# Performance work log

Measured on AMD Instinct MI355X. Metric: run time of the kernel, lower is better.

The kernel has to match this reference:

```python
import jax, jax.numpy as jnp
import numpy as np

EPS = 1e-06
GROUPS = ((0, 16), (16, 32), (32, 64))


def setup_inputs() -> dict:
    key = jax.random.key(0)
    k1, k2, k3 = jax.random.split(key, 3)
    B, C, H, W = 32, 64, 128, 128
    x = jax.random.normal(k1, (B, C, H, W), dtype=jnp.float32)
    # stands in for Beta(0.1, 0.1) sample in the torch module
    lmda = jax.random.uniform(k2, (B, 1, 1, 1), dtype=jnp.float32)
    perm = jax.random.permutation(k3, B).astype(jnp.int32)
    return {"x": x, "lmda": lmda, "perm": perm}


def _lower_median(a, axis):
    # torch.median returns the lower of the two middle values for even n
    n = a.shape[axis]
    s = jnp.sort(a, axis=axis)
    return jax.lax.slice_in_dim(s, (n - 1) // 2, (n - 1) // 2 + 1, axis=axis)


def _group_mix(xg, lmda, perm):
    B, Cg, H, W = xg.shape
    mu = jax.lax.stop_gradient(jnp.mean(xg, axis=(2, 3), keepdims=True))
    var = jnp.var(xg, axis=(2, 3), keepdims=True, ddof=1)  # torch unbiased var
    sig = jax.lax.stop_gradient(jnp.sqrt(var + EPS))
    x_normed = (xg - mu) / sig

    med = jax.lax.stop_gradient(_lower_median(_lower_median(xg, 2), 3))  # [B,Cg,1,1]

    flat = xg.reshape(B, Cg, H * W)
    gram = jnp.einsum('bci,bdi->bcd', flat, flat) / (H * W + EPS)
    gram = jax.lax.stop_gradient(gram) + (0.001 + 1e-06) * jnp.eye(Cg, dtype=xg.dtype)

    w, v = jnp.linalg.eigh(gram)
    inv_sqrt = 1.0 / jnp.sqrt(w + EPS)
    whitening = jnp.einsum('bij,bj,bkj->bik', v, inv_sqrt, v)  # [B,Cg,Cg]

    xw = jnp.einsum('bcd,bdn->bcn', whitening, flat - mu.reshape(B, Cg, 1))
    xw = xw.reshape(B, Cg, H, W)

    gram_mix = xw * lmda + xw[perm] * (1.0 - lmda)
    med_mix = med * lmda + med[perm] * (1.0 - lmda)
    return x_normed * gram_mix + med_mix


def reference(x, lmda, perm):
    outs = [_group_mix(x[:, s:e], lmda, perm) for s, e in GROUPS]
    return jnp.concatenate(outs, axis=1)
```

## Files before the change

### kernel.cpp

```cpp
#include <hip/hip_runtime.h>
#include <hip/hip_fp16.h>

#define HWPIX 16384

typedef _Float16 h2 __attribute__((ext_vector_type(2)));
typedef int v2i __attribute__((ext_vector_type(2)));
typedef float f2 __attribute__((ext_vector_type(2)));
typedef float f4 __attribute__((ext_vector_type(4)));


#define TPAD 130

template<int J>
__device__ inline unsigned shfl_xor_u(unsigned v, int lane) {
  if constexpr (J == 1)
    return (unsigned)__builtin_amdgcn_mov_dpp((int)v, 0xB1, 0xF, 0xF, true);
  else if constexpr (J == 2)
    return (unsigned)__builtin_amdgcn_mov_dpp((int)v, 0x4E, 0xF, 0xF, true);
  else if constexpr (J == 4)
    return (unsigned)__builtin_amdgcn_ds_swizzle((int)v, 0x101F);
  else if constexpr (J == 8)
    return (unsigned)__builtin_amdgcn_ds_swizzle((int)v, 0x201F);
  else if constexpr (J == 16)
    return (unsigned)__builtin_amdgcn_ds_swizzle((int)v, 0x401F);
  else {
#if __has_builtin(__builtin_amdgcn_permlane32_swap)
    v2i r = __builtin_amdgcn_permlane32_swap((int)v, (int)v, false, false);
    return (lane & 32) ? (unsigned)r[0] : (unsigned)r[1];
#else
    return (unsigned)__shfl_xor((int)v, 32);
#endif
  }
}

__device__ inline unsigned pk_min(unsigned a, unsigned b) {
  h2 x = __builtin_bit_cast(h2, a), y = __builtin_bit_cast(h2, b);
  return __builtin_bit_cast(unsigned, __builtin_elementwise_min(x, y));
}
__device__ inline unsigned pk_max(unsigned a, unsigned b) {
  h2 x = __builtin_bit_cast(h2, a), y = __builtin_bit_cast(h2, b);
  return __builtin_bit_cast(unsigned, __builtin_elementwise_max(x, y));
}

template<int CTRL>
__device__ inline unsigned dppmax(unsigned m) {
  unsigned t = (unsigned)__builtin_amdgcn_update_dpp((int)m, (int)m, CTRL, 0xF, 0xF, false);
  return pk_max(m, t);
}

template<int K, int J, int Q>
__device__ inline void bstep(unsigned (&v0)[Q], unsigned (&v1)[Q], const int lane) {
  const bool sel0 = (((lane & J) == 0) == ((lane & K) == 0));
  const int i1 = lane + 64;
  const bool sel1 = (((i1 & J) == 0) == ((i1 & K) == 0));
  unsigned pv[Q];
  #pragma unroll
  for (int q = 0; q < Q; ++q) pv[q] = shfl_xor_u<J>(v0[q], lane);
  #pragma unroll
  for (int q = 0; q < Q; ++q)
    v0[q] = sel0 ? pk_min(v0[q], pv[q]) : pk_max(v0[q], pv[q]);
  #pragma unroll
  for (int q = 0; q < Q; ++q) pv[q] = shfl_xor_u<J>(v1[q], lane);
  #pragma unroll
  for (int q = 0; q < Q; ++q)
    v1[q] = sel1 ? pk_min(v1[q], pv[q]) : pk_max(v1[q], pv[q]);
  if constexpr (J > 1) bstep<K, J / 2, Q>(v0, v1, lane);
}

template<int Q>
__device__ inline void median128h_low(unsigned (&v0)[Q], unsigned (&v1)[Q],
                                      unsigned (&m)[Q], const int lane) {
  bstep<2, 1, Q>(v0, v1, lane);
  bstep<4, 2, Q>(v0, v1, lane);
  bstep<8, 4, Q>(v0, v1, lane);
  bstep<16, 8, Q>(v0, v1, lane);
  bstep<32, 16, Q>(v0, v1, lane);
  bstep<64, 32, Q>(v0, v1, lane);
  #pragma unroll
  for (int q = 0; q < Q; ++q) m[q] = pk_min(v0[q], v1[q]);
  #pragma unroll
  for (int q = 0; q < Q; ++q) m[q] = dppmax<0x111>(m[q]);
  #pragma unroll
  for (int q = 0; q < Q; ++q) m[q] = dppmax<0x112>(m[q]);
  #pragma unroll
  for (int q = 0; q < Q; ++q) m[q] = dppmax<0x114>(m[q]);
  #pragma unroll
  for (int q = 0; q < Q; ++q) m[q] = dppmax<0x118>(m[q]);
  #pragma unroll
  for (int q = 0; q < Q; ++q) m[q] = dppmax<0x142>(m[q]);
  #pragma unroll
  for (int q = 0; q < Q; ++q) m[q] = dppmax<0x143>(m[q]);
}

template<int CTRL>
__device__ inline float fmax_dpp(float m) {
  float t = __builtin_bit_cast(float,
      __builtin_amdgcn_update_dpp(__builtin_bit_cast(int, m),
                                  __builtin_bit_cast(int, m), CTRL, 0xF, 0xF, false));
  return fmaxf(m, t);
}

__device__ inline float median128f_low(float v0, float v1, const int lane) {
  #pragma unroll
  for (int k = 2; k <= 64; k <<= 1) {
    #pragma unroll
    for (int j = k >> 1; j > 0; j >>= 1) {
      const bool sel0 = (((lane & j) == 0) == ((lane & k) == 0));
      const int i1 = lane + 64;
      const bool sel1 = (((i1 & j) == 0) == ((i1 & k) == 0));
      float pv = __shfl_xor(v0, j);
      v0 = sel0 ? fminf(v0, pv) : fmaxf(v0, pv);
      float pw = __shfl_xor(v1, j);
      v1 = sel1 ? fminf(v1, pw) : fmaxf(v1, pw);
    }
  }
  float m = fminf(v0, v1);
  m = fmax_dpp<0x111>(m); m = fmax_dpp<0x112>(m); m = fmax_dpp<0x114>(m);
  m = fmax_dpp<0x118>(m); m = fmax_dpp<0x142>(m); m = fmax_dpp<0x143>(m);
  return m;
}

__global__ __launch_bounds__(512) void stats_kernel(const float* __restrict__ x,
                                                    float* __restrict__ med) {
  __shared__ __half tile[128 * TPAD];
  __shared__ float colmed[128];

  const int bc = blockIdx.x;
  const int tid = threadIdx.x;
  const float* xp = x + (size_t)bc * HWPIX;

  #pragma unroll
  for (int j = 0; j < 8; ++j) {
    int v = tid + j * 512;
    int h = v >> 5;
    int w = (v & 31) * 4;
    float4 val = *reinterpret_cast<const float4*>(xp + (size_t)v * 4);
    __half2* dst = reinterpret_cast<__half2*>(&tile[h * TPAD + w]);
    dst[0] = __floats2half2_rn(val.x, val.y);
    dst[1] = __floats2half2_rn(val.z, val.w);
  }
  __syncthreads();

  const int lane = tid & 63;
  const int wid  = tid >> 6;
  {
    const int w = wid * 16;
    unsigned v0[8], v1[8], m[8];
    #pragma unroll
    for (int q = 0; q < 8; ++q) {
      v0[q] = *reinterpret_cast<const unsigned*>(&tile[lane * TPAD + w + 2 * q]);
      v1[q] = *reinterpret_cast<const unsigned*>(&tile[(lane + 64) * TPAD + w + 2 * q]);
    }
    median128h_low<8>(v0, v1, m, lane);
    if (lane == 63) {
      #pragma unroll
      for (int q = 0; q < 8; ++q) {
        h2 mv = __builtin_bit_cast(h2, m[q]);
        colmed[w + 2 * q]     = (float)mv.x;
        colmed[w + 2 * q + 1] = (float)mv.y;
      }
    }
  }
  __syncthreads();
  if (wid == 0) {
    float m = median128f_low(colmed[lane], colmed[lane + 64], lane);
    if (lane == 63) med[bc] = m;
  }
}

template<int CG>
__global__ __launch_bounds__(256) void gram_kernel(const float* __restrict__ x,
                                                   float* __restrict__ gpart,
                                                   float* __restrict__ rspart) {
  constexpr int QT   = CG / 4;
  constexpr int TPG  = QT * QT;
  constexpr int PQ   = 256 / TPG;
  constexpr int SUBP = 256 / PQ;
  constexpr int THR  = 256 / CG;
  __shared__ float tile[CG][260];

  const int b = blockIdx.z;
  const int g = blockIdx.y;
  const int s    = (CG == 16) ? g * 16  : 32;
  const int goff = (CG == 16) ? g * 256 : 512;
  const int chunk = blockIdx.x;
  const int k0 = chunk * 1024;
  const int tid = threadIdx.x;
  const int pq = tid / TPG;
  const int t  = tid % TPG;
  const int ty = t / QT, tx = t % QT;
  const int r0 = ty * 4, c0 = tx * 4;
  const int rrow = tid / THR;
  const int rseg = tid % THR;

  const float* xb = x + (((size_t)(b * 64 + s)) << 14) + k0;
  float acc[4][4] = {};
  float rsum = 0.f;

  for (int sc = 0; sc < 4; ++sc) {
    #pragma unroll
    for (int v = tid; v < CG * 64; v += 256) {
      int r = v >> 6;
      int p4 = (v & 63) * 4;
      *reinterpret_cast<float4*>(&tile[r][p4]) =
          *reinterpret_cast<const float4*>(xb + ((size_t)r << 14) + sc * 256 + p4);
    }
    __syncthreads();
    const int pb0 = pq * SUBP;
    #pragma unroll
    for (int p = pb0; p < pb0 + SUBP; p += 4) {
      float4 a[4], bb[4];
      #pragma unroll
      for (int i = 0; i < 4; ++i) a[i]  = *reinterpret_cast<const float4*>(&tile[r0 + i][p]);
      #pragma unroll
      for (int i = 0; i < 4; ++i) bb[i] = *reinterpret_cast<const float4*>(&tile[c0 + i][p]);
      #pragma unroll
      for (int i = 0; i < 4; ++i)
        #pragma unroll
        for (int j = 0; j < 4; ++j)
          acc[i][j] += a[i].x * bb[j].x + a[i].y * bb[j].y +
                       a[i].z * bb[j].z + a[i].w * bb[j].w;
    }
    #pragma unroll
    for (int i = 0; i < CG / 4; ++i) {
      const float4 v = *reinterpret_cast<const float4*>(&tile[rrow][rseg * CG + i * 4]);
      rsum += v.x + v.y + v.z + v.w;
    }
    __syncthreads();
  }

  #pragma unroll
  for (int j = 1; j < THR; j <<= 1) rsum += __shfl_xor(rsum, j);
  if (rseg == 0) rspart[chunk * 2048 + b * 64 + s + rrow] = rsum;

  float* scratch = reinterpret_cast<float*>(tile);
  #pragma unroll
  for (int i = 0; i < 4; ++i)
    #pragma unroll
    for (int j = 0; j < 4; ++j)
      scratch[(t * PQ + pq) * 16 + i * 4 + j] = acc[i][j];
  __syncthreads();
  if (pq == 0) {
    float* gp = gpart + (size_t)(chunk * 32 + b) * 1536 + goff;
    #pragma unroll
    for (int i = 0; i < 4; ++i)
      #pragma unroll
      for (int j = 0; j < 4; ++j) {
        float v = 0.f;
        for (int q = 0; q < PQ; ++q) v += scratch[(t * PQ + q) * 16 + i * 4 + j];
        gp[(r0 + i) * CG + (c0 + j)] = v;
      }
  }
}

template<int CG>
__device__ __forceinline__ void ns_impl(const float* __restrict__ gpart,
                                        const float* __restrict__ rspart,
                                        float* __restrict__ mu,
                                        float* __restrict__ rsig,
                                        float* __restrict__ wht,
                                        const int b, const int g, char* smem) {
  constexpr int NE = CG * CG;
  constexpr int PADC = CG + 4;
  constexpr int MS = CG * PADC;
  float* Y0 = (float*)smem;
  float* Z0 = Y0 + MS;
  float* Y1 = Z0 + MS;
  float* Z1 = Y1 + MS;
  float* T  = Z1 + MS;
  float* red = T + MS;

  const int s    = (CG == 16) ? g * 16  : 32;
  const int goff = (CG == 16) ? g * 256 : 512;
  const int tid = threadIdx.x;
  const float invHW = (float)(1.0 / (16384.0 + 1e-6));

  for (int e = tid; e < NE; e += 256) {
    int r = e / CG, c = e % CG;
    float v = 0.f;
    #pragma unroll
    for (int ch = 0; ch < 16; ++ch)
      v += gpart[(size_t)(ch * 32 + b) * 1536 + goff + e];
    T[r * PADC + c] = v;
  }
  __syncthreads();

  if (tid < CG) {
    float rs = 0.f;
    #pragma unroll
    for (int ch = 0; ch < 16; ++ch) rs += rspart[ch * 2048 + b * 64 + s + tid];
    const float diag = T[tid * PADC + tid];
    const float mean = rs * (1.0f / HWPIX);
    const float var = (diag - rs * mean) / (float)(HWPIX - 1);
    mu[b * 64 + s + tid] = mean;
    rsig[b * 64 + s + tid] = rsqrtf(var + 1e-6f);
  }
  __syncthreads();

  float ssq = 0.f;
  for (int e = tid; e < NE; e += 256) {
    int r = e / CG, c = e % CG;
    float v = T[r * PADC + c] * invHW + ((r == c) ? 0.001002f : 0.0f);
    T[r * PADC + c] = v;
    ssq += v * v;
  }
  red[tid] = ssq;
  __syncthreads();
  for (int off = 128; off > 0; off >>= 1) {
    if (tid < off) red[tid] += red[tid + off];
    __syncthreads();
  }
  const float cn = sqrtf(red[0]);
  const float icn = 1.0f / cn;
  for (int e = tid; e < NE; e += 256) {
    int r = e / CG, c = e % CG;
    Y0[r * PADC + c] = T[r * PADC + c] * icn;
    Z0[r * PADC + c] = (r == c) ? 1.0f : 0.0f;
  }
  __syncthreads();

  constexpr int ACT = NE / 4;
  const int r  = tid / (CG / 4);
  const int c0 = (tid % (CG / 4)) * 4;

  for (int it = 0; it < 12; ++it) {
    float* Yi = (it & 1) ? Y1 : Y0;
    float* Zi = (it & 1) ? Z1 : Z0;
    float* Yo = (it & 1) ? Y0 : Y1;
    float* Zo = (it & 1) ? Z0 : Z1;
    if (tid < ACT) {
      float ax = 0.f, ay = 0.f, az = 0.f, aw = 0.f;
      #pragma unroll
      for (int k = 0; k < CG; ++k) {
        float zr = Zi[r * PADC + k];
        const float4 yk = *reinterpret_cast<const float4*>(&Yi[k * PADC + c0]);
        ax += zr * yk.x; ay += zr * yk.y; az += zr * yk.z; aw += zr * yk.w;
      }
      float4 tv;
      tv.x = ((r == c0 + 0) ? 3.f : 0.f) - ax;
      tv.y = ((r == c0 + 1) ? 3.f : 0.f) - ay;
      tv.z = ((r == c0 + 2) ? 3.f : 0.f) - az;
      tv.w = ((r == c0 + 3) ? 3.f : 0.f) - aw;
      *reinterpret_cast<float4*>(&T[r * PADC + c0]) = tv;
    }
    __syncthreads();
    if (tid < ACT) {
      float yx = 0.f, yy = 0.f, yz = 0.f, yw = 0.f;
      float zx = 0.f, zy = 0.f, zz = 0.f, zw = 0.f;
      #pragma unroll
      for (int k = 0; k < CG; ++k) {
        float yr = Yi[r * PADC + k];
        float tr = T[r * PADC + k];
        const float4 tk = *reinterpret_cast<const float4*>(&T[k * PADC + c0]);
        const float4 zk = *reinterpret_cast<const float4*>(&Zi[k * PADC + c0]);
        yx += yr * tk.x; yy += yr * tk.y; yz += yr * tk.z; yw += yr * tk.w;
        zx += tr * zk.x; zy += tr * zk.y; zz += tr * zk.z; zw += tr * zk.w;
      }
      *reinterpret_cast<float4*>(&Yo[r * PADC + c0]) =
          make_float4(0.5f * yx, 0.5f * yy, 0.5f * yz, 0.5f * yw);
      *reinterpret_cast<float4*>(&Zo[r * PADC + c0]) =
          make_float4(0.5f * zx, 0.5f * zy, 0.5f * zz, 0.5f * zw);
    }
    __syncthreads();
  }

  const float wscale = rsqrtf(cn);
  for (int e = tid; e < NE; e += 256) {
    int r2 = e / CG, c2 = e % CG;
    wht[b * 1536 + goff + e] = Z0[r2 * PADC + c2] * wscale;
  }
}

__global__ __launch_bounds__(256) void ns_all(const float* __restrict__ gpart,
                                              const float* __restrict__ rspart,
                                              float* __restrict__ mu,
                                              float* __restrict__ rsig,
                                              float* __restrict__ wht) {
  __shared__ __align__(16) char smem[5 * 32 * 36 * 4 + 1024];
  const int bid = blockIdx.x;
  if (bid < 64) ns_impl<16>(gpart, rspart, mu, rsig, wht, bid >> 1, bid & 1, smem);
  else          ns_impl<32>(gpart, rspart, mu, rsig, wht, bid - 64, 0, smem);
}

__global__ __launch_bounds__(256, 2) void apply16(
    const float* __restrict__ x, const float* __restrict__ lmda,
    const int* __restrict__ perm, const float* __restrict__ mu,
    const float* __restrict__ rsig, const float* __restrict__ med,
    const float* __restrict__ wht, float* __restrict__ out) {
  __shared__ float W1[256], W2[256];
  __shared__ float mu1[16], mu2[16], rs1[16], mm[16];

  const int b = blockIdx.z;
  const int g = blockIdx.y;
  const int s = g * 16, goff = g * 256;
  const int tid = threadIdx.x;
  const int pb = perm[b];
  const float lam = lmda[b];
  const float oml = 1.0f - lam;

  if (tid < 256) {
    W1[tid] = wht[b  * 1536 + goff + tid] * lam;
    W2[tid] = wht[pb * 1536 + goff + tid] * oml;
  }
  if (tid < 16) {
    int ch1 = b * 64 + s + tid, ch2 = pb * 64 + s + tid;
    mu1[tid] = mu[ch1];
    mu2[tid] = mu[ch2];
    rs1[tid] = rsig[ch1];
    mm[tid]  = lam * med[ch1] + oml * med[ch2];
  }
  __syncthreads();

  const int p = blockIdx.x * 1024 + tid * 4;
  const float* xb1 = x + (((size_t)(b  * 64 + s)) << 14) + p;
  const float* xb2 = x + (((size_t)(pb * 64 + s)) << 14) + p;
  float* ob = out + (((size_t)(b * 64 + s)) << 14) + p;

  f4 xv1[16], xv2[16];
  #pragma unroll
  for (int d = 0; d < 16; ++d) xv1[d] = *reinterpret_cast<const f4*>(xb1 + ((size_t)d << 14));
  #pragma unroll
  for (int d = 0; d < 16; ++d) xv2[d] = *reinterpret_cast<const f4*>(xb2 + ((size_t)d << 14));
  #pragma unroll
  for (int d = 0; d < 16; ++d) { xv1[d] -= mu1[d]; xv2[d] -= mu2[d]; }

  f4 acc[16] = {};
  #pragma unroll
  for (int d = 0; d < 16; ++d) {
    #pragma unroll
    for (int c = 0; c < 16; ++c) {
      acc[c] += W1[d * 16 + c] * xv1[d];
      acc[c] += W2[d * 16 + c] * xv2[d];
    }
  }
  #pragma unroll
  for (int c = 0; c < 16; ++c) {
    f4 v = xv1[c] * rs1[c] * acc[c] + mm[c];
    __builtin_nontemporal_store(v, reinterpret_cast<f4*>(ob + ((size_t)c << 14)));
  }
}

__global__ __launch_bounds__(256, 2) void apply32(
    const float* __restrict__ x, const float* __restrict__ lmda,
    const int* __restrict__ perm, const float* __restrict__ mu,
    const float* __restrict__ rsig, const float* __restrict__ med,
    const float* __restrict__ wht, float* __restrict__ out) {
  __shared__ float W1[1024], W2[1024];
  __shared__ float mu1[32], mu2[32], rs1[32], mm[32];

  const int b = blockIdx.z;
  const int tid = threadIdx.x;
  const int pb = perm[b];
  const float lam = lmda[b];
  const float oml = 1.0f - lam;

  for (int e = tid; e < 1024; e += 256) {
    W1[e] = wht[b  * 1536 + 512 + e] * lam;
    W2[e] = wht[pb * 1536 + 512 + e] * oml;
  }
  if (tid < 32) {
    int ch1 = b * 64 + 32 + tid, ch2 = pb * 64 + 32 + tid;
    mu1[tid] = mu[ch1];
    mu2[tid] = mu[ch2];
    rs1[tid] = rsig[ch1];
    mm[tid]  = lam * med[ch1] + oml * med[ch2];
  }
  __syncthreads();

  const int p = blockIdx.x * 512 + tid * 2;
  const float* xb1 = x + (((size_t)(b  * 64 + 32)) << 14) + p;
  const float* xb2 = x + (((size_t)(pb * 64 + 32)) << 14) + p;
  float* ob = out + (((size_t)(b * 64 + 32)) << 14) + p;

  f2 xv1[32], xv2[32];
  #pragma unroll
  for (int d = 0; d < 32; ++d) xv1[d] = *reinterpret_cast<const f2*>(xb1 + ((size_t)d << 14));
  #pragma unroll
  for (int d = 0; d < 32; ++d) xv2[d] = *reinterpret_cast<const f2*>(xb2 + ((size_t)d << 14));
  #pragma unroll
  for (int d = 0; d < 32; ++d) { xv1[d] -= mu1[d]; xv2[d] -= mu2[d]; }

  f2 acc[32] = {};
  #pragma unroll
  for (int d = 0; d < 32; ++d) {
    #pragma unroll
    for (int c = 0; c < 32; ++c) {
      acc[c] += W1[d * 32 + c] * xv1[d];
      acc[c] += W2[d * 32 + c] * xv2[d];
    }
  }
  #pragma unroll
  for (int c = 0; c < 32; ++c) {
    f2 v = xv1[c] * rs1[c] * acc[c] + mm[c];
    __builtin_nontemporal_store(v, reinterpret_cast<f2*>(ob + ((size_t)c << 14)));
  }
}

extern "C" void kernel_launch(void* const* d_in, const int* in_sizes, int n_in,
                              void* d_out, int out_size, void* d_ws, size_t ws_size,
                              hipStream_t stream) {
  const float* x    = (const float*)d_in[0];
  const float* lmda = (const float*)d_in[1];
  const int*   perm = (const int*)d_in[2];
  float* out = (float*)d_out;
  float* ws  = (float*)d_ws;

  float* mu     = ws;
  float* rsig   = ws + 2048;
  float* med    = ws + 4096;
  float* wht    = ws + 6144;
  float* rspart = ws + 55296;
  float* gpart  = ws + 88064;

  gram_kernel<16><<<dim3(16, 2, 32), 256, 0, stream>>>(x, gpart, rspart);
  gram_kernel<32><<<dim3(16, 1, 32), 256, 0, stream>>>(x, gpart, rspart);

  stats_kernel<<<2048, 512, 0, stream>>>(x, med);

  ns_all<<<96, 256, 0, stream>>>(gpart, rspart, mu, rsig, wht);

  apply16<<<dim3(16, 2, 32), 256, 0, stream>>>(x, lmda, perm, mu, rsig, med, wht, out);
  apply32<<<dim3(32, 1, 32), 256, 0, stream>>>(x, lmda, perm, mu, rsig, med, wht, out);
}
```

Baseline: 247.2 us.

## Load median columns directly into registers and halve apply16 pixels per thread

```diff
diff --git a/kernel.cpp b/kernel.cpp
--- a/kernel.cpp
+++ b/kernel.cpp
@@ -8,8 +8,6 @@
 typedef float f2 __attribute__((ext_vector_type(2)));
 typedef float f4 __attribute__((ext_vector_type(4)));
 
-
-#define TPAD 130
 
 template<int J>
 __device__ inline unsigned shfl_xor_u(unsigned v, int lane) {
@@ -42,6 +40,11 @@
   return __builtin_bit_cast(unsigned, __builtin_elementwise_max(x, y));
 }
 
+__device__ inline unsigned pack2(float x, float y) {
+  h2 p = {(_Float16)x, (_Float16)y};
+  return __builtin_bit_cast(unsigned, p);
+}
+
 template<int CTRL>
 __device__ inline unsigned dppmax(unsigned m) {
   unsigned t = (unsigned)__builtin_amdgcn_update_dpp((int)m, (int)m, CTRL, 0xF, 0xF, false);
@@ -120,44 +123,41 @@
   return m;
 }
 
-__global__ __launch_bounds__(512) void stats_kernel(const float* __restrict__ x,
+__global__ __launch_bounds__(256) void stats_kernel(const float* __restrict__ x,
                                                     float* __restrict__ med) {
-  __shared__ __half tile[128 * TPAD];
   __shared__ float colmed[128];
 
   const int bc = blockIdx.x;
   const int tid = threadIdx.x;
-  const float* xp = x + (size_t)bc * HWPIX;
-
-  #pragma unroll
-  for (int j = 0; j < 8; ++j) {
-    int v = tid + j * 512;
-    int h = v >> 5;
-    int w = (v & 31) * 4;
-    float4 val = *reinterpret_cast<const float4*>(xp + (size_t)v * 4);
-    __half2* dst = reinterpret_cast<__half2*>(&tile[h * TPAD + w]);
-    dst[0] = __floats2half2_rn(val.x, val.y);
-    dst[1] = __floats2half2_rn(val.z, val.w);
-  }
-  __syncthreads();
-
   const int lane = tid & 63;
   const int wid  = tid >> 6;
-  {
-    const int w = wid * 16;
+  const float* rowA = x + (size_t)bc * HWPIX + (size_t)lane * 128 + wid * 32;
+  const float* rowB = rowA + (size_t)64 * 128;
+
+  unsigned a[16], b[16];
+  #pragma unroll
+  for (int i = 0; i < 8; ++i) {
+    f4 va = *reinterpret_cast<const f4*>(rowA + i * 4);
+    f4 vb = *reinterpret_cast<const f4*>(rowB + i * 4);
+    a[2 * i]     = pack2(va.x, va.y);
+    a[2 * i + 1] = pack2(va.z, va.w);
+    b[2 * i]     = pack2(vb.x, vb.y);
+    b[2 * i + 1] = pack2(vb.z, vb.w);
+  }
+
+  #pragma unroll
+  for (int t = 0; t < 2; ++t) {
     unsigned v0[8], v1[8], m[8];
     #pragma unroll
-    for (int q = 0; q < 8; ++q) {
-      v0[q] = *reinterpret_cast<const unsigned*>(&tile[lane * TPAD + w + 2 * q]);
-      v1[q] = *reinterpret_cast<const unsigned*>(&tile[(lane + 64) * TPAD + w + 2 * q]);
-    }
+    for (int q = 0; q < 8; ++q) { v0[q] = a[t * 8 + q]; v1[q] = b[t * 8 + q]; }
     median128h_low<8>(v0, v1, m, lane);
     if (lane == 63) {
+      const int base = wid * 32 + t * 16;
       #pragma unroll
       for (int q = 0; q < 8; ++q) {
         h2 mv = __builtin_bit_cast(h2, m[q]);
-        colmed[w + 2 * q]     = (float)mv.x;
-        colmed[w + 2 * q + 1] = (float)mv.y;
+        colmed[base + 2 * q]     = (float)mv.x;
+        colmed[base + 2 * q + 1] = (float)mv.y;
       }
     }
   }
@@ -382,7 +382,7 @@
   else          ns_impl<32>(gpart, rspart, mu, rsig, wht, bid - 64, 0, smem);
 }
 
-__global__ __launch_bounds__(256, 2) void apply16(
+__global__ __launch_bounds__(256, 4) void apply16(
     const float* __restrict__ x, const float* __restrict__ lmda,
     const int* __restrict__ perm, const float* __restrict__ mu,
     const float* __restrict__ rsig, const float* __restrict__ med,
@@ -411,20 +411,20 @@
   }
   __syncthreads();
 
-  const int p = blockIdx.x * 1024 + tid * 4;
+  const int p = blockIdx.x * 512 + tid * 2;
   const float* xb1 = x + (((size_t)(b  * 64 + s)) << 14) + p;
   const float* xb2 = x + (((size_t)(pb * 64 + s)) << 14) + p;
   float* ob = out + (((size_t)(b * 64 + s)) << 14) + p;
 
-  f4 xv1[16], xv2[16];
-  #pragma unroll
-  for (int d = 0; d < 16; ++d) xv1[d] = *reinterpret_cast<const f4*>(xb1 + ((size_t)d << 14));
-  #pragma unroll
-  for (int d = 0; d < 16; ++d) xv2[d] = *reinterpret_cast<const f4*>(xb2 + ((size_t)d << 14));
+  f2 xv1[16], xv2[16];
+  #pragma unroll
+  for (int d = 0; d < 16; ++d) xv1[d] = *reinterpret_cast<const f2*>(xb1 + ((size_t)d << 14));
+  #pragma unroll
+  for (int d = 0; d < 16; ++d) xv2[d] = *reinterpret_cast<const f2*>(xb2 + ((size_t)d << 14));
   #pragma unroll
   for (int d = 0; d < 16; ++d) { xv1[d] -= mu1[d]; xv2[d] -= mu2[d]; }
 
-  f4 acc[16] = {};
+  f2 acc[16] = {};
   #pragma unroll
   for (int d = 0; d < 16; ++d) {
     #pragma unroll
@@ -435,8 +435,8 @@
   }
   #pragma unroll
   for (int c = 0; c < 16; ++c) {
-    f4 v = xv1[c] * rs1[c] * acc[c] + mm[c];
-    __builtin_nontemporal_store(v, reinterpret_cast<f4*>(ob + ((size_t)c << 14)));
+    f2 v = xv1[c] * rs1[c] * acc[c] + mm[c];
+    __builtin_nontemporal_store(v, reinterpret_cast<f2*>(ob + ((size_t)c << 14)));
   }
 }
 
@@ -515,10 +515,10 @@
   gram_kernel<16><<<dim3(16, 2, 32), 256, 0, stream>>>(x, gpart, rspart);
   gram_kernel<32><<<dim3(16, 1, 32), 256, 0, stream>>>(x, gpart, rspart);
 
-  stats_kernel<<<2048, 512, 0, stream>>>(x, med);
+  stats_kernel<<<2048, 256, 0, stream>>>(x, med);
 
   ns_all<<<96, 256, 0, stream>>>(gpart, rspart, mu, rsig, wht);
 
-  apply16<<<dim3(16, 2, 32), 256, 0, stream>>>(x, lmda, perm, mu, rsig, med, wht, out);
+  apply16<<<dim3(32, 2, 32), 256, 0, stream>>>(x, lmda, perm, mu, rsig, med, wht, out);
   apply32<<<dim3(32, 1, 32), 256, 0, stream>>>(x, lmda, perm, mu, rsig, med, wht, out);
 }
```

Result: faster. 224.0 us (-9.4%).
